# Performance work log

Measured on AMD Instinct MI355X. Metric: run time of the kernel, lower is better.

Reference implementation:

```python
import jax, jax.numpy as jnp
import numpy as np

N = 1048576  # total points
B = 64       # number of clouds in batch
D = 64       # feature dim


def _make_lengths():
    rng = np.random.RandomState(0)
    w = rng.rand(B) + 0.5
    lengths = np.floor(w / w.sum() * N).astype(np.int64)
    lengths[-1] += N - lengths.sum()  # make lengths sum exactly to N
    return lengths


def setup_inputs() -> dict:
    key = jax.random.key(0)
    x = jax.random.normal(key, (N, D), dtype=jnp.float32)
    lengths_np = _make_lengths()
    segment_ids = jnp.asarray(np.repeat(np.arange(B, dtype=np.int64), lengths_np))
    lengths = jnp.asarray(lengths_np)
    return {"x": x, "segment_ids": segment_ids, "lengths": lengths}


def reference(x, segment_ids, lengths):
    # fused segmented mean: one pass over x instead of B separate mean kernels
    sums = jax.ops.segment_sum(x, segment_ids, num_segments=B)  # [B, D]
    return sums / lengths.astype(x.dtype)[:, None]
```

## Files before the change

kernel.cpp:

```cpp
#include <hip/hip_runtime.h>


#define D 64
#define ROWS_PER_BLOCK 512
#define NTHREADS 256

typedef float f32x4 __attribute__((ext_vector_type(4)));

__global__ __launch_bounds__(NTHREADS) void seg_sum_kernel(
    const float* __restrict__ x,
    const int*   __restrict__ seg,
    float*       __restrict__ out,
    int n_rows)
{
    __shared__ float lacc[2][D];
    __shared__ int sBoundary, sNb;

    const int tid = threadIdx.x;
    const int r0  = blockIdx.x * ROWS_PER_BLOCK;
    if (r0 >= n_rows) return;
    int r1 = r0 + ROWS_PER_BLOCK;
    if (r1 > n_rows) r1 = n_rows;

    const int col     = (tid & 15) * 4;
    const int rowlane = tid >> 4;

    const int s0 = seg[r0];
    const int sN = seg[r1 - 1];

    for (int i = tid; i < 2 * D; i += NTHREADS) ((float*)lacc)[i] = 0.0f;
    if (tid == 0) { sBoundary = r1; sNb = 0; }
    __syncthreads();

    int boundary = r1, nb = 0;
    if (s0 != sN) {
        for (int i = r0 + 1 + tid; i < r1; i += NTHREADS) {
            if (seg[i] != seg[i - 1]) { atomicAdd(&sNb, 1); atomicMin(&sBoundary, i); }
        }
        __syncthreads();
        boundary = sBoundary;
        nb       = sNb;
    }

    if (nb <= 1) {
        f32x4 a0 = {0.f, 0.f, 0.f, 0.f};
        f32x4 a1 = {0.f, 0.f, 0.f, 0.f};

        if (boundary >= r1 && (r1 - r0) == ROWS_PER_BLOCK) {
            const float* p = x + (size_t)(r0 + rowlane) * D + col;
            f32x4 t0 = {0.f,0.f,0.f,0.f}, t1 = {0.f,0.f,0.f,0.f};
            f32x4 t2 = {0.f,0.f,0.f,0.f}, t3 = {0.f,0.f,0.f,0.f};
            #pragma unroll
            for (int it = 0; it < 8; ++it) {
                const int base = it * 64;
                t0 += *reinterpret_cast<const f32x4*>(p + (base +  0) * D);
                t1 += *reinterpret_cast<const f32x4*>(p + (base + 16) * D);
                t2 += *reinterpret_cast<const f32x4*>(p + (base + 32) * D);
                t3 += *reinterpret_cast<const f32x4*>(p + (base + 48) * D);
            }
            a0 = (t0 + t1) + (t2 + t3);
        } else {
            for (int r = r0 + rowlane; r < r1; r += 16) {
                const f32x4 v = *reinterpret_cast<const f32x4*>(
                    x + (size_t)r * D + col);
                if (r < boundary) { a0 += v; } else { a1 += v; }
            }
        }

        atomicAdd(&lacc[0][col + 0], a0.x);
        atomicAdd(&lacc[0][col + 1], a0.y);
        atomicAdd(&lacc[0][col + 2], a0.z);
        atomicAdd(&lacc[0][col + 3], a0.w);
        if (boundary < r1) {
            atomicAdd(&lacc[1][col + 0], a1.x);
            atomicAdd(&lacc[1][col + 1], a1.y);
            atomicAdd(&lacc[1][col + 2], a1.z);
            atomicAdd(&lacc[1][col + 3], a1.w);
        }
        __syncthreads();
        if (tid < D) {
            atomicAdd(&out[(size_t)s0 * D + tid], lacc[0][tid]);
            if (boundary < r1)
                atomicAdd(&out[(size_t)sN * D + tid], lacc[1][tid]);
        }
    } else {
        f32x4 a = {0.f, 0.f, 0.f, 0.f};
        int cur = -1;
        for (int r = r0 + rowlane; r < r1; r += 16) {
            const int s = seg[r];
            const f32x4 v = *reinterpret_cast<const f32x4*>(x + (size_t)r * D + col);
            if (s != cur) {
                if (cur >= 0) {
                    atomicAdd(&out[(size_t)cur * D + col + 0], a.x);
                    atomicAdd(&out[(size_t)cur * D + col + 1], a.y);
                    atomicAdd(&out[(size_t)cur * D + col + 2], a.z);
                    atomicAdd(&out[(size_t)cur * D + col + 3], a.w);
                }
                a = {0.f, 0.f, 0.f, 0.f};
                cur = s;
            }
            a += v;
        }
        if (cur >= 0) {
            atomicAdd(&out[(size_t)cur * D + col + 0], a.x);
            atomicAdd(&out[(size_t)cur * D + col + 1], a.y);
            atomicAdd(&out[(size_t)cur * D + col + 2], a.z);
            atomicAdd(&out[(size_t)cur * D + col + 3], a.w);
        }
    }
}

__global__ __launch_bounds__(NTHREADS) void seg_div_kernel(
    const int* __restrict__ len,
    float*     __restrict__ out,
    int total)
{
    const int i = blockIdx.x * blockDim.x + threadIdx.x;
    if (i < total) {
        out[i] = out[i] / (float)len[i >> 6];
    }
}

extern "C" void kernel_launch(void* const* d_in, const int* in_sizes, int n_in,
                              void* d_out, int out_size, void* d_ws, size_t ws_size,
                              hipStream_t stream) {
    const float* x   = (const float*)d_in[0];
    const int*   seg = (const int*)d_in[1];
    const int*   len = (const int*)d_in[2];
    float*       out = (float*)d_out;

    const int n_rows = in_sizes[1];
    const int B      = in_sizes[2];
    const int total  = B * D;

    hipMemsetAsync(out, 0, (size_t)total * sizeof(float), stream);

    const int grid = (n_rows + ROWS_PER_BLOCK - 1) / ROWS_PER_BLOCK;
    seg_sum_kernel<<<grid, NTHREADS, 0, stream>>>(x, seg, out, n_rows);

    const int grid2 = (total + NTHREADS - 1) / NTHREADS;
    seg_div_kernel<<<grid2, NTHREADS, 0, stream>>>(len, out, total);
}
```

Before: 374.4 us.

## Derive block segment boundaries from lengths via wave prefix scan, prefetch rows early

Each block now reads the lengths array and computes segment start offsets with a wavefront shuffle prefix scan, then uses ballots to find the first segment and any boundary inside the block. This replaces scanning segment_ids with shared-memory atomics and the extra barrier that scan needed. The first eight row loads are issued before the boundary logic so memory latency overlaps the scan. It assumes segment_ids are sorted and consistent with lengths; when B exceeds 64 it falls back to reading segment ids.

```diff
diff --git a/kernel.cpp b/kernel.cpp
--- a/kernel.cpp
+++ b/kernel.cpp
@@ -10,11 +10,11 @@
 __global__ __launch_bounds__(NTHREADS) void seg_sum_kernel(
     const float* __restrict__ x,
     const int*   __restrict__ seg,
+    const int*   __restrict__ len,
     float*       __restrict__ out,
-    int n_rows)
+    int n_rows, int B)
 {
     __shared__ float lacc[2][D];
-    __shared__ int sBoundary, sNb;
 
     const int tid = threadIdx.x;
     const int r0  = blockIdx.x * ROWS_PER_BLOCK;
@@ -24,54 +24,95 @@
 
     const int col     = (tid & 15) * 4;
     const int rowlane = tid >> 4;
+    const int lane    = tid & 63;
 
-    const int s0 = seg[r0];
-    const int sN = seg[r1 - 1];
+    const bool full = (r1 - r0) == ROWS_PER_BLOCK;
 
-    for (int i = tid; i < 2 * D; i += NTHREADS) ((float*)lacc)[i] = 0.0f;
-    if (tid == 0) { sBoundary = r1; sNb = 0; }
-    __syncthreads();
+    int mylen = 0;
+    if (B <= 64 && lane < B) mylen = len[lane];
 
-    int boundary = r1, nb = 0;
-    if (s0 != sN) {
-        for (int i = r0 + 1 + tid; i < r1; i += NTHREADS) {
-            if (seg[i] != seg[i - 1]) { atomicAdd(&sNb, 1); atomicMin(&sBoundary, i); }
+    const float* p = x + (size_t)(r0 + rowlane) * D + col;
+    f32x4 w0{}, w1{}, w2{}, w3{}, w4{}, w5{}, w6{}, w7{};
+    if (full) {
+        w0 = *(const f32x4*)(p + (size_t)0 * 16 * D);
+        w1 = *(const f32x4*)(p + (size_t)1 * 16 * D);
+        w2 = *(const f32x4*)(p + (size_t)2 * 16 * D);
+        w3 = *(const f32x4*)(p + (size_t)3 * 16 * D);
+        w4 = *(const f32x4*)(p + (size_t)4 * 16 * D);
+        w5 = *(const f32x4*)(p + (size_t)5 * 16 * D);
+        w6 = *(const f32x4*)(p + (size_t)6 * 16 * D);
+        w7 = *(const f32x4*)(p + (size_t)7 * 16 * D);
+    }
+
+    int s0, nb, boundary = r1;
+    if (B <= 64) {
+        int incl = mylen;
+        #pragma unroll
+        for (int d = 1; d < 64; d <<= 1) {
+            const int t = __shfl_up(incl, d, 64);
+            if (lane >= d) incl += t;
         }
-        __syncthreads();
-        boundary = sBoundary;
-        nb       = sNb;
+        const int o_beg = incl - mylen;
+        s0 = __popcll(__ballot(o_beg <= r0)) - 1;
+        const unsigned long long mb = __ballot(o_beg > r0 && o_beg < r1);
+        nb = __popcll(mb);
+        if (nb) boundary = __shfl(o_beg, (int)(__ffsll((long long)mb) - 1), 64);
+    } else {
+        s0 = seg[r0];
+        nb = (seg[r1 - 1] != s0) ? 2 : 0;
     }
 
     if (nb <= 1) {
         f32x4 a0 = {0.f, 0.f, 0.f, 0.f};
         f32x4 a1 = {0.f, 0.f, 0.f, 0.f};
 
-        if (boundary >= r1 && (r1 - r0) == ROWS_PER_BLOCK) {
-            const float* p = x + (size_t)(r0 + rowlane) * D + col;
-            f32x4 t0 = {0.f,0.f,0.f,0.f}, t1 = {0.f,0.f,0.f,0.f};
-            f32x4 t2 = {0.f,0.f,0.f,0.f}, t3 = {0.f,0.f,0.f,0.f};
+        if (full && nb == 0) {
+            f32x4 t0 = w0, t1 = w1, t2 = w2, t3 = w3;
+            t0 += w4; t1 += w5; t2 += w6; t3 += w7;
             #pragma unroll
-            for (int it = 0; it < 8; ++it) {
-                const int base = it * 64;
-                t0 += *reinterpret_cast<const f32x4*>(p + (base +  0) * D);
-                t1 += *reinterpret_cast<const f32x4*>(p + (base + 16) * D);
-                t2 += *reinterpret_cast<const f32x4*>(p + (base + 32) * D);
-                t3 += *reinterpret_cast<const f32x4*>(p + (base + 48) * D);
+            for (int it = 1; it < 4; ++it) {
+                const float* q = p + (size_t)it * 128 * D;
+                const f32x4 v0 = *(const f32x4*)(q + (size_t)0 * 16 * D);
+                const f32x4 v1 = *(const f32x4*)(q + (size_t)1 * 16 * D);
+                const f32x4 v2 = *(const f32x4*)(q + (size_t)2 * 16 * D);
+                const f32x4 v3 = *(const f32x4*)(q + (size_t)3 * 16 * D);
+                const f32x4 v4 = *(const f32x4*)(q + (size_t)4 * 16 * D);
+                const f32x4 v5 = *(const f32x4*)(q + (size_t)5 * 16 * D);
+                const f32x4 v6 = *(const f32x4*)(q + (size_t)6 * 16 * D);
+                const f32x4 v7 = *(const f32x4*)(q + (size_t)7 * 16 * D);
+                t0 += v0; t1 += v1; t2 += v2; t3 += v3;
+                t0 += v4; t1 += v5; t2 += v6; t3 += v7;
             }
             a0 = (t0 + t1) + (t2 + t3);
+        } else if (full) {
+            const int rbase = r0 + rowlane;
+            if (rbase +   0 < boundary) a0 += w0; else a1 += w0;
+            if (rbase +  16 < boundary) a0 += w1; else a1 += w1;
+            if (rbase +  32 < boundary) a0 += w2; else a1 += w2;
+            if (rbase +  48 < boundary) a0 += w3; else a1 += w3;
+            if (rbase +  64 < boundary) a0 += w4; else a1 += w4;
+            if (rbase +  80 < boundary) a0 += w5; else a1 += w5;
+            if (rbase +  96 < boundary) a0 += w6; else a1 += w6;
+            if (rbase + 112 < boundary) a0 += w7; else a1 += w7;
+            #pragma unroll 8
+            for (int r = rbase + 128; r < r1; r += 16) {
+                const f32x4 v = *(const f32x4*)(x + (size_t)r * D + col);
+                if (r < boundary) { a0 += v; } else { a1 += v; }
+            }
         } else {
             for (int r = r0 + rowlane; r < r1; r += 16) {
-                const f32x4 v = *reinterpret_cast<const f32x4*>(
-                    x + (size_t)r * D + col);
+                const f32x4 v = *(const f32x4*)(x + (size_t)r * D + col);
                 if (r < boundary) { a0 += v; } else { a1 += v; }
             }
         }
 
+        for (int i = tid; i < 2 * D; i += NTHREADS) ((float*)lacc)[i] = 0.0f;
+        __syncthreads();
         atomicAdd(&lacc[0][col + 0], a0.x);
         atomicAdd(&lacc[0][col + 1], a0.y);
         atomicAdd(&lacc[0][col + 2], a0.z);
         atomicAdd(&lacc[0][col + 3], a0.w);
-        if (boundary < r1) {
+        if (nb) {
             atomicAdd(&lacc[1][col + 0], a1.x);
             atomicAdd(&lacc[1][col + 1], a1.y);
             atomicAdd(&lacc[1][col + 2], a1.z);
@@ -80,15 +121,15 @@
         __syncthreads();
         if (tid < D) {
             atomicAdd(&out[(size_t)s0 * D + tid], lacc[0][tid]);
-            if (boundary < r1)
-                atomicAdd(&out[(size_t)sN * D + tid], lacc[1][tid]);
+            if (nb)
+                atomicAdd(&out[(size_t)(s0 + 1) * D + tid], lacc[1][tid]);
         }
     } else {
         f32x4 a = {0.f, 0.f, 0.f, 0.f};
         int cur = -1;
         for (int r = r0 + rowlane; r < r1; r += 16) {
             const int s = seg[r];
-            const f32x4 v = *reinterpret_cast<const f32x4*>(x + (size_t)r * D + col);
+            const f32x4 v = *(const f32x4*)(x + (size_t)r * D + col);
             if (s != cur) {
                 if (cur >= 0) {
                     atomicAdd(&out[(size_t)cur * D + col + 0], a.x);
@@ -136,7 +177,7 @@
     hipMemsetAsync(out, 0, (size_t)total * sizeof(float), stream);
 
     const int grid = (n_rows + ROWS_PER_BLOCK - 1) / ROWS_PER_BLOCK;
-    seg_sum_kernel<<<grid, NTHREADS, 0, stream>>>(x, seg, out, n_rows);
+    seg_sum_kernel<<<grid, NTHREADS, 0, stream>>>(x, seg, len, out, n_rows, B);
 
     const int grid2 = (total + NTHREADS - 1) / NTHREADS;
     seg_div_kernel<<<grid2, NTHREADS, 0, stream>>>(len, out, total);
```

Result: faster. 363.1 us (-3.0%).
